# Performance work log

Measured on AMD Instinct MI355X. Metric: run time of the kernel, lower is better.

## Reference

```python
import jax, jax.numpy as jnp
import numpy as np

TAU = 0.07
EPS = 1e-12  # matches torch F.normalize default eps


def setup_inputs() -> dict:
    key = jax.random.key(0)
    k1, k2 = jax.random.split(key)
    B, C, H, W, K = 4, 256, 256, 256, 19
    feat = jax.random.normal(k1, (B, C, H, W), dtype=jnp.float32)
    # binary ground-truth one-hot-ish masks; gt.eq(1) selects positives
    gt = jax.random.randint(k2, (B, K, H, W), 0, 2).astype(jnp.float32)
    return {"feat": feat, "gt": gt}


def _l2norm(x, axis):
    n = jnp.sqrt(jnp.sum(x * x, axis=axis, keepdims=True))
    return x / jnp.maximum(n, EPS)


def reference(feat, gt):
    # feat: [B,C,H,W], gt: [B,K,H,W] binary
    pos = (gt == 1.0).astype(feat.dtype)              # [B,K,H,W]
    fnorm = _l2norm(feat, axis=1)                     # per-pixel L2 normalize over C
    # scatter-add normalized features into class prototypes
    k0 = jnp.einsum('bkhw,bchw->kc', pos, fnorm)      # [K,C]
    k0n = _l2norm(k0, axis=1)                         # [K,C]
    # prototype-vs-pixel similarities, softmax over classes
    logits = jnp.einsum('kc,bchw->bkhw', k0n, fnorm) / TAU  # [B,K,H,W]
    logp = jax.nn.log_softmax(logits, axis=1)
    num_pos = jnp.sum(pos)
    loss = -jnp.sum(pos * logp) / num_pos
    return loss
```

## Files before the change

### kernel.cpp

```cpp
#include <hip/hip_runtime.h>
#include <math.h>

namespace {
constexpr int Bn = 4;
constexpr int Cn = 256;
constexpr int Kn = 19;
constexpr int HW = 256 * 256;
constexpr int P  = Bn * HW;
constexpr float TAUv = 0.07f;
constexpr float EPSv = 1e-12f;

constexpr int K0_OFF   = 0;
constexpr int K0NT_OFF = 4864;
constexpr int SUMS_OFF = 9728;
constexpr int PART_OFF = 9984;
constexpr int P1_GRID  = 512;
constexpr int ZERO_N   = 9730;
}

__global__ __launch_bounds__(256) void gc_init(float* __restrict__ ws) {
  int i = blockIdx.x * 256 + threadIdx.x;
  if (i < ZERO_N) ws[i] = 0.0f;
}

__global__ __launch_bounds__(256) void gc_phase1(const float* __restrict__ feat,
                                                 const float* __restrict__ gt,
                                                 float* __restrict__ ws) {
  __shared__ float tile[64 * 256];
  float* k0   = ws + K0_OFF;
  float* part = ws + PART_OFF;

  const int t    = threadIdx.x;
  const int lane = t & 63;
  const int wv   = t >> 6;

  float acc[Kn];
#pragma unroll
  for (int k = 0; k < Kn; k++) acc[k] = 0.0f;

  for (int tid = blockIdx.x; tid < P / 64; tid += gridDim.x) {
    const int p0  = tid << 6;
    const int b   = p0 >> 16;
    const int hw0 = p0 & (HW - 1);
    const float* fb = feat + (size_t)b * (Cn * HW) + hw0 + lane;
    const float* gb = gt   + (size_t)b * (Kn * HW) + hw0 + lane;

    __syncthreads();

    float ss = 0.0f;
#pragma unroll 8
    for (int j = 0; j < 64; j++) {
      const int c = (wv << 6) + j;
      const float v = fb[(size_t)c * HW];
      ss += v * v;
      tile[(lane << 8) + (c ^ (lane & 31))] = v;
    }
    part[(blockIdx.x << 8) + t] = ss;

    unsigned my_mask = 0;
#pragma unroll
    for (int k = 0; k < Kn; k++)
      my_mask |= (gb[(size_t)k * HW] == 1.0f) ? (1u << k) : 0u;

    __syncthreads();

    float fss = 0.0f;
#pragma unroll
    for (int q = 0; q < 4; q++) fss += part[(blockIdx.x << 8) + (q << 6) + lane];
    const float my_rn = 1.0f / fmaxf(sqrtf(fss), EPSv);

#pragma unroll 4
    for (int p = 0; p < 64; p++) {
      const float rp = __shfl(my_rn, p);
      unsigned mp = (unsigned)__shfl((int)my_mask, p);
      mp = __builtin_amdgcn_readfirstlane(mp);
      const float fv = tile[(p << 8) + (t ^ (p & 31))] * rp;
#pragma unroll
      for (int k = 0; k < Kn; k++)
        if (mp & (1u << k)) acc[k] += fv;
    }
  }

#pragma unroll
  for (int k = 0; k < Kn; k++) atomicAdd(&k0[k * 256 + t], acc[k]);
}

__global__ __launch_bounds__(256) void gc_phase2(float* __restrict__ ws) {
  const float* k0 = ws + K0_OFF;
  float* k0nT = ws + K0NT_OFF;
  const int lane = threadIdx.x & 63;
  const int wv   = threadIdx.x >> 6;
  for (int r = wv; r < Kn; r += 4) {
    float s = 0.0f;
#pragma unroll
    for (int j = 0; j < 4; j++) {
      const float v = k0[r * 256 + (j << 6) + lane];
      s += v * v;
    }
#pragma unroll
    for (int off = 32; off > 0; off >>= 1) s += __shfl_down(s, off);
    s = __shfl(s, 0);
    const float rn = 1.0f / fmaxf(sqrtf(s), EPSv);
#pragma unroll
    for (int j = 0; j < 4; j++) {
      const int c = (j << 6) + lane;
      k0nT[c * Kn + r] = k0[r * 256 + c] * rn;
    }
  }
}

__global__ __launch_bounds__(256) void gc_phase3(const float* __restrict__ feat,
                                                 const float* __restrict__ gt,
                                                 float* __restrict__ ws) {
  const float* k0nT = ws + K0NT_OFF;
  float* sums = ws + SUMS_OFF;

  const int t   = threadIdx.x;
  const int pix = (blockIdx.x << 8) + t;
  const int b   = pix >> 16;
  const int hw  = pix & (HW - 1);
  const float* fb = feat + (size_t)b * (Cn * HW) + hw;

  float dot[Kn];
#pragma unroll
  for (int k = 0; k < Kn; k++) dot[k] = 0.0f;
  float ss = 0.0f;

#pragma unroll 2
  for (int c = 0; c < Cn; c++) {
    const float f = fb[(size_t)c * HW];
    ss += f * f;
#pragma unroll
    for (int k = 0; k < Kn; k++) dot[k] = fmaf(f, k0nT[c * Kn + k], dot[k]);
  }

  const float sc = 1.0f / (fmaxf(sqrtf(ss), EPSv) * TAUv);
  float mx = -1e30f;
#pragma unroll
  for (int k = 0; k < Kn; k++) { dot[k] *= sc; mx = fmaxf(mx, dot[k]); }
  float se = 0.0f;
#pragma unroll
  for (int k = 0; k < Kn; k++) se += __expf(dot[k] - mx);
  const float lse = __logf(se) + mx;

  const float* gb = gt + (size_t)b * (Kn * HW) + hw;
  float lsum = 0.0f;
  float npos = 0.0f;
#pragma unroll
  for (int k = 0; k < Kn; k++) {
    if (gb[(size_t)k * HW] == 1.0f) { lsum += lse - dot[k]; npos += 1.0f; }
  }

#pragma unroll
  for (int off = 32; off > 0; off >>= 1) {
    lsum += __shfl_down(lsum, off);
    npos += __shfl_down(npos, off);
  }
  if ((t & 63) == 0) {
    atomicAdd(&sums[0], lsum);
    atomicAdd(&sums[1], npos);
  }
}

__global__ void gc_finalize(const float* __restrict__ ws, float* __restrict__ out) {
  if (threadIdx.x == 0 && blockIdx.x == 0)
    out[0] = ws[SUMS_OFF] / ws[SUMS_OFF + 1];
}

extern "C" void kernel_launch(void* const* d_in, const int* in_sizes, int n_in,
                              void* d_out, int out_size, void* d_ws, size_t ws_size,
                              hipStream_t stream) {
  const float* feat = (const float*)d_in[0];
  const float* gt   = (const float*)d_in[1];
  float* ws  = (float*)d_ws;
  float* out = (float*)d_out;

  gc_init<<<dim3((ZERO_N + 255) / 256), dim3(256), 0, stream>>>(ws);
  gc_phase1<<<dim3(P1_GRID), dim3(256), 0, stream>>>(feat, gt, ws);
  gc_phase2<<<dim3(1), dim3(256), 0, stream>>>(ws);
  gc_phase3<<<dim3(P / 256), dim3(256), 0, stream>>>(feat, gt, ws);
  gc_finalize<<<dim3(1), dim3(64), 0, stream>>>(ws, out);
}
```

Baseline: 638.8 us.

## Restructure prototype accumulation and similarity loops for less memory traffic

Phase 1 now keeps the per-pixel sum-of-squares partials and the normalization/mask pairs in shared memory, where before they went through global workspace and cross-lane shuffles. Only the first wave loads the gt masks, and the per-class conditional adds become branchless FMAs with a 0/1 weight. Phase 1 gets a two-blocks-per-SM launch bound. Phase 3 loads 16 channels at a time into registers and reads the normalized prototypes row-major in contiguous runs, which raises memory-level parallelism and lets the prototype loads become wide uniform loads. The cost is higher register pressure in phase 3 and extra FMAs in phase 1.

After: 652.8 us. 1.02x slower.

```diff
diff --git a/kernel.cpp b/kernel.cpp
--- a/kernel.cpp
+++ b/kernel.cpp
@@ -11,9 +11,8 @@
 constexpr float EPSv = 1e-12f;
 
 constexpr int K0_OFF   = 0;
-constexpr int K0NT_OFF = 4864;
+constexpr int K0N_OFF  = 4864;
 constexpr int SUMS_OFF = 9728;
-constexpr int PART_OFF = 9984;
 constexpr int P1_GRID  = 512;
 constexpr int ZERO_N   = 9730;
 }
@@ -23,12 +22,12 @@
   if (i < ZERO_N) ws[i] = 0.0f;
 }
 
-__global__ __launch_bounds__(256) void gc_phase1(const float* __restrict__ feat,
-                                                 const float* __restrict__ gt,
-                                                 float* __restrict__ ws) {
+__global__ __launch_bounds__(256, 2) void gc_phase1(const float* __restrict__ feat,
+                                                    const float* __restrict__ gt,
+                                                    float* __restrict__ k0) {
   __shared__ float tile[64 * 256];
-  float* k0   = ws + K0_OFF;
-  float* part = ws + PART_OFF;
+  __shared__ float part[256];
+  __shared__ float2 pm[64];
 
   const int t    = threadIdx.x;
   const int lane = t & 63;
@@ -43,7 +42,6 @@
     const int b   = p0 >> 16;
     const int hw0 = p0 & (HW - 1);
     const float* fb = feat + (size_t)b * (Cn * HW) + hw0 + lane;
-    const float* gb = gt   + (size_t)b * (Kn * HW) + hw0 + lane;
 
     __syncthreads();
 
@@ -55,29 +53,37 @@
       ss += v * v;
       tile[(lane << 8) + (c ^ (lane & 31))] = v;
     }
-    part[(blockIdx.x << 8) + t] = ss;
+    part[t] = ss;
 
     unsigned my_mask = 0;
+    if (wv == 0) {
+      const float* gb = gt + (size_t)b * (Kn * HW) + hw0 + lane;
 #pragma unroll
-    for (int k = 0; k < Kn; k++)
-      my_mask |= (gb[(size_t)k * HW] == 1.0f) ? (1u << k) : 0u;
+      for (int k = 0; k < Kn; k++)
+        my_mask |= (gb[(size_t)k * HW] == 1.0f) ? (1u << k) : 0u;
+    }
 
     __syncthreads();
 
-    float fss = 0.0f;
-#pragma unroll
-    for (int q = 0; q < 4; q++) fss += part[(blockIdx.x << 8) + (q << 6) + lane];
-    const float my_rn = 1.0f / fmaxf(sqrtf(fss), EPSv);
+    if (wv == 0) {
+      const float fss = part[lane] + part[64 + lane] + part[128 + lane] + part[192 + lane];
+      const float rn = 1.0f / fmaxf(sqrtf(fss), EPSv);
+      pm[lane] = make_float2(rn, __uint_as_float(my_mask));
+    }
+
+    __syncthreads();
 
 #pragma unroll 4
     for (int p = 0; p < 64; p++) {
-      const float rp = __shfl(my_rn, p);
-      unsigned mp = (unsigned)__shfl((int)my_mask, p);
-      mp = __builtin_amdgcn_readfirstlane(mp);
+      const float2 pr = pm[p];
+      const float rp = __uint_as_float(__builtin_amdgcn_readfirstlane(__float_as_uint(pr.x)));
+      const unsigned m = __builtin_amdgcn_readfirstlane(__float_as_uint(pr.y));
       const float fv = tile[(p << 8) + (t ^ (p & 31))] * rp;
 #pragma unroll
-      for (int k = 0; k < Kn; k++)
-        if (mp & (1u << k)) acc[k] += fv;
+      for (int k = 0; k < Kn; k++) {
+        const float w = (float)((m >> k) & 1u);
+        acc[k] = fmaf(fv, w, acc[k]);
+      }
     }
   }
 
@@ -85,9 +91,8 @@
   for (int k = 0; k < Kn; k++) atomicAdd(&k0[k * 256 + t], acc[k]);
 }
 
-__global__ __launch_bounds__(256) void gc_phase2(float* __restrict__ ws) {
-  const float* k0 = ws + K0_OFF;
-  float* k0nT = ws + K0NT_OFF;
+__global__ __launch_bounds__(256) void gc_phase2(const float* __restrict__ k0,
+                                                 float* __restrict__ k0n) {
   const int lane = threadIdx.x & 63;
   const int wv   = threadIdx.x >> 6;
   for (int r = wv; r < Kn; r += 4) {
@@ -104,17 +109,15 @@
 #pragma unroll
     for (int j = 0; j < 4; j++) {
       const int c = (j << 6) + lane;
-      k0nT[c * Kn + r] = k0[r * 256 + c] * rn;
+      k0n[r * 256 + c] = k0[r * 256 + c] * rn;
     }
   }
 }
 
 __global__ __launch_bounds__(256) void gc_phase3(const float* __restrict__ feat,
                                                  const float* __restrict__ gt,
-                                                 float* __restrict__ ws) {
-  const float* k0nT = ws + K0NT_OFF;
-  float* sums = ws + SUMS_OFF;
-
+                                                 const float* __restrict__ k0n,
+                                                 float* __restrict__ sums) {
   const int t   = threadIdx.x;
   const int pix = (blockIdx.x << 8) + t;
   const int b   = pix >> 16;
@@ -126,12 +129,20 @@
   for (int k = 0; k < Kn; k++) dot[k] = 0.0f;
   float ss = 0.0f;
 
-#pragma unroll 2
-  for (int c = 0; c < Cn; c++) {
-    const float f = fb[(size_t)c * HW];
-    ss += f * f;
+  for (int c0 = 0; c0 < Cn; c0 += 16) {
+    float f[16];
 #pragma unroll
-    for (int k = 0; k < Kn; k++) dot[k] = fmaf(f, k0nT[c * Kn + k], dot[k]);
+    for (int j = 0; j < 16; j++) f[j] = fb[(size_t)(c0 + j) * HW];
+#pragma unroll
+    for (int j = 0; j < 16; j++) ss = fmaf(f[j], f[j], ss);
+#pragma unroll
+    for (int k = 0; k < Kn; k++) {
+      const float* row = k0n + k * 256 + c0;
+      float d = dot[k];
+#pragma unroll
+      for (int j = 0; j < 16; j++) d = fmaf(f[j], row[j], d);
+      dot[k] = d;
+    }
   }
 
   const float sc = 1.0f / (fmaxf(sqrtf(ss), EPSv) * TAUv);
@@ -162,9 +173,9 @@
   }
 }
 
-__global__ void gc_finalize(const float* __restrict__ ws, float* __restrict__ out) {
+__global__ void gc_finalize(const float* __restrict__ sums, float* __restrict__ out) {
   if (threadIdx.x == 0 && blockIdx.x == 0)
-    out[0] = ws[SUMS_OFF] / ws[SUMS_OFF + 1];
+    out[0] = sums[0] / sums[1];
 }
 
 extern "C" void kernel_launch(void* const* d_in, const int* in_sizes, int n_in,
@@ -175,9 +186,13 @@
   float* ws  = (float*)d_ws;
   float* out = (float*)d_out;
 
+  float* k0   = ws + K0_OFF;
+  float* k0n  = ws + K0N_OFF;
+  float* sums = ws + SUMS_OFF;
+
   gc_init<<<dim3((ZERO_N + 255) / 256), dim3(256), 0, stream>>>(ws);
-  gc_phase1<<<dim3(P1_GRID), dim3(256), 0, stream>>>(feat, gt, ws);
-  gc_phase2<<<dim3(1), dim3(256), 0, stream>>>(ws);
-  gc_phase3<<<dim3(P / 256), dim3(256), 0, stream>>>(feat, gt, ws);
-  gc_finalize<<<dim3(1), dim3(64), 0, stream>>>(ws, out);
+  gc_phase1<<<dim3(P1_GRID), dim3(256), 0, stream>>>(feat, gt, k0);
+  gc_phase2<<<dim3(1), dim3(256), 0, stream>>>(k0, k0n);
+  gc_phase3<<<dim3(P / 256), dim3(256), 0, stream>>>(feat, gt, k0n, sums);
+  gc_finalize<<<dim3(1), dim3(64), 0, stream>>>(sums, out);
 }
```
